# Kernel optimization log

Hardware: AMD Instinct MI355X
Metric: run time of the kernel (lower is better)

## Reference

```python
import jax, jax.numpy as jnp
import numpy as np

H, DH = 16, 64  # heads, dim_head (inner_dim = 1024)
VARIANCE_CONSTANT = 1.0


def setup_inputs() -> dict:
    key = jax.random.key(0)
    ks = jax.random.split(key, 6)
    b, n, m, dim = 8, 4096, 64, 1024
    inner = H * DH
    x = jax.random.normal(ks[0], (b, n, dim), dtype=jnp.float32)
    latents = jax.random.normal(ks[1], (b, m, dim), dtype=jnp.float32)
    mask = jax.random.randint(ks[2], (b, n), 0, 2).astype(bool)  # True = masked out
    sd = 1.0 / np.sqrt(dim)
    Wq = jax.random.normal(ks[3], (inner, dim), dtype=jnp.float32) * sd
    Wkv = jax.random.normal(ks[4], (2 * inner, dim), dtype=jnp.float32) * sd
    Wout = jax.random.normal(ks[5], (dim, inner), dtype=jnp.float32) * sd
    return {"x": x, "latents": latents, "mask": mask, "Wq": Wq, "Wkv": Wkv, "Wout": Wout}


def _split_heads(t):  # b n (h d) -> b h n d
    b, n, _ = t.shape
    return t.reshape(b, n, H, DH).transpose(0, 2, 1, 3)


def reference(x, latents, mask, Wq, Wkv, Wout):
    b, n, dim = x.shape
    scale = DH ** -0.5
    q = latents @ Wq.T                      # b m inner
    k, v = jnp.split(x @ Wkv.T, 2, axis=-1)  # b n inner each
    q = _split_heads(q) * scale             # b h m d
    k = _split_heads(k)                     # b h n d
    v = _split_heads(v)
    sim = jnp.einsum('bhid,bhjd->bhij', q, k)  # b h m n
    max_neg = -jnp.finfo(sim.dtype).max
    sim = jnp.where(mask[:, None, None, :], max_neg, sim)
    sim_new = sim - jax.lax.stop_gradient(sim.max(axis=-1, keepdims=True))
    # cross-query (dim=-2) unbiased variance -> std over latents, shape b h n
    std = jnp.sqrt(jnp.var(sim_new, axis=-2, ddof=1) + 1e-4)
    std = jnp.where(mask[:, None, :], VARIANCE_CONSTANT, std)
    loss_variance = jnp.mean(jax.nn.relu(VARIANCE_CONSTANT - std))
    attn = jax.nn.softmax(sim_new, axis=-1)
    out = jnp.einsum('bhij,bhjd->bhid', attn, v)         # b h m d
    out = out.transpose(0, 2, 1, 3).reshape(b, -1, H * DH)  # b m inner
    out = out @ Wout.T                                    # b m dim
    return out, loss_variance
```

## Files before the change

kernel.cpp:

```cpp
#include <hip/hip_runtime.h>


using u16 = unsigned short;
typedef short bf16x8_t __attribute__((ext_vector_type(8)));
typedef float f32x4_t __attribute__((ext_vector_type(4)));

__device__ __forceinline__ u16 f2bf(float f) {
    union { float f; unsigned u; } v; v.f = f;
    unsigned r = v.u + 0x7fffu + ((v.u >> 16) & 1u);
    return (u16)(r >> 16);
}

template <typename T> __device__ __forceinline__ T cvt_out(float v);
template <> __device__ __forceinline__ float cvt_out<float>(float v) { return v; }
template <> __device__ __forceinline__ u16   cvt_out<u16>(float v)   { return f2bf(v); }

__device__ __forceinline__ void cp16(const void* g, void* l) {
    __builtin_amdgcn_global_load_lds((const __attribute__((address_space(1))) unsigned int*)g,
                                     (__attribute__((address_space(3))) unsigned int*)l, 16, 0, 0);
}

__global__ void cvt_bf16(const float* __restrict__ src, u16* __restrict__ dst,
                         int n4, float scale) {
    int i = blockIdx.x * 256 + threadIdx.x;
    if (i >= n4) return;
    float4 v = ((const float4*)src)[i];
    ushort4 o;
    o.x = f2bf(v.x * scale); o.y = f2bf(v.y * scale);
    o.z = f2bf(v.z * scale); o.w = f2bf(v.w * scale);
    ((ushort4*)dst)[i] = o;
}

template <typename OutT, bool SWIZ>
__global__ __launch_bounds__(256) void gemm_bt(const u16* __restrict__ A,
                                               const u16* __restrict__ B,
                                               OutT* __restrict__ C,
                                               int M, int N, int K) {
    __shared__ __align__(16) u16 As[128 * 64];
    __shared__ __align__(16) u16 Bs[128 * 64];
    const int tid = threadIdx.x;
    const int wid = tid >> 6, lane = tid & 63;
    int bx = blockIdx.x, by = blockIdx.y;
    if (SWIZ) {
        int fid = blockIdx.y * 16 + blockIdx.x;
        int xcd = fid & 7, l = fid >> 3;
        int s = l >> 6, w = l & 63;
        int sm = s & 3, sn = s >> 2;
        by = xcd * 32 + sm * 8 + (w >> 3);
        bx = sn * 8 + (w & 7);
    }
    const int bm = by * 128, bn = bx * 128;
    const int srow = lane >> 3;
    const int scol = ((lane & 7) ^ srow) * 8;
    const int frow = lane & 15;
    const int wr = (wid >> 1) * 64, wc = (wid & 1) * 64;

    f32x4_t acc[4][4];
#pragma unroll
    for (int i = 0; i < 4; ++i)
#pragma unroll
        for (int j = 0; j < 4; ++j) acc[i][j] = (f32x4_t){0.f, 0.f, 0.f, 0.f};

    for (int k0 = 0; k0 < K; k0 += 64) {
#pragma unroll
        for (int t = 0; t < 4; ++t) {
            const int c = wid * 4 + t;
            const int r = c * 8 + srow;
            cp16(A + (size_t)(bm + r) * K + k0 + scol, As + c * 512);
            cp16(B + (size_t)(bn + r) * K + k0 + scol, Bs + c * 512);
        }
        __syncthreads();
#pragma unroll
        for (int ks = 0; ks < 2; ++ks) {
            const int grp = (((ks * 4 + (lane >> 4)) ^ (frow & 7)) * 8);
            bf16x8_t af[4], bfv[4];
#pragma unroll
            for (int i = 0; i < 4; ++i) {
                af[i]  = *(const bf16x8_t*)(As + (wr + i * 16 + frow) * 64 + grp);
                bfv[i] = *(const bf16x8_t*)(Bs + (wc + i * 16 + frow) * 64 + grp);
            }
#pragma unroll
            for (int i = 0; i < 4; ++i)
#pragma unroll
                for (int j = 0; j < 4; ++j)
                    acc[i][j] = __builtin_amdgcn_mfma_f32_16x16x32_bf16(af[i], bfv[j], acc[i][j], 0, 0, 0);
        }
        __syncthreads();
    }
    const int cr = (lane >> 4) * 4, cc = lane & 15;
#pragma unroll
    for (int i = 0; i < 4; ++i)
#pragma unroll
        for (int j = 0; j < 4; ++j) {
            size_t base = (size_t)(bm + wr + i * 16 + cr) * N + (bn + wc + j * 16 + cc);
#pragma unroll
            for (int r = 0; r < 4; ++r)
                C[base + (size_t)r * N] = cvt_out<OutT>(acc[i][j][r]);
        }
}

__global__ __launch_bounds__(256, 1) void attn_max(const u16* __restrict__ q,
                                                   const u16* __restrict__ kv,
                                                   const int* __restrict__ mask,
                                                   float* __restrict__ Mg) {
    const int c = blockIdx.x & 3, bh = blockIdx.x >> 2, b = bh >> 4, h = bh & 15;
    const int tid = threadIdx.x, wid = tid >> 6, lane = tid & 63;
    const int frow = lane & 15, cr = (lane >> 4) * 4;
    const int srow = lane >> 3, scol = ((lane & 7) ^ srow) * 8;

    __shared__ __align__(16) u16 qs[64 * 64];
    __shared__ __align__(16) u16 ks[256 * 64];
    __shared__ float maskf[256];
    __shared__ float Mpart[4][64];

    const size_t kvbase = (size_t)b * 4096 * 2048 + (size_t)h * 64;

#pragma unroll
    for (int t = 0; t < 2; ++t) {
        int cq = wid * 2 + t;
        int r = cq * 8 + srow;
        cp16(q + (size_t)(b * 64 + r) * 1024 + h * 64 + scol, qs + cq * 512);
    }

    float mloc[16];
#pragma unroll
    for (int i = 0; i < 16; ++i) mloc[i] = -3.0e38f;

    for (int sc = 0; sc < 4; ++sc) {
        const int j0 = c * 1024 + sc * 256;
        __syncthreads();
#pragma unroll
        for (int t = 0; t < 8; ++t) {
            int cs = wid * 8 + t;
            int r = cs * 8 + srow;
            cp16(kv + kvbase + (size_t)(j0 + r) * 2048 + scol, ks + cs * 512);
        }
        maskf[tid] = (mask[b * 4096 + j0 + tid] != 0) ? 1.f : 0.f;
        __syncthreads();

        f32x4_t sacc[4][4];
#pragma unroll
        for (int i = 0; i < 4; ++i)
#pragma unroll
            for (int j = 0; j < 4; ++j) sacc[i][j] = (f32x4_t){0.f, 0.f, 0.f, 0.f};
#pragma unroll
        for (int ks2 = 0; ks2 < 2; ++ks2) {
            const int grp = (((ks2 * 4 + (lane >> 4)) ^ (frow & 7)) * 8);
            bf16x8_t af[4], bfv[4];
#pragma unroll
            for (int i = 0; i < 4; ++i) {
                af[i]  = *(const bf16x8_t*)(qs + (i * 16 + frow) * 64 + grp);
                bfv[i] = *(const bf16x8_t*)(ks + (wid * 64 + i * 16 + frow) * 64 + grp);
            }
#pragma unroll
            for (int i = 0; i < 4; ++i)
#pragma unroll
                for (int j = 0; j < 4; ++j)
                    sacc[i][j] = __builtin_amdgcn_mfma_f32_16x16x32_bf16(af[i], bfv[j], sacc[i][j], 0, 0, 0);
        }
#pragma unroll
        for (int nt = 0; nt < 4; ++nt) {
            const int jl = wid * 64 + nt * 16 + frow;
            if (maskf[jl] < 0.5f) {
#pragma unroll
                for (int mt = 0; mt < 4; ++mt)
#pragma unroll
                    for (int r = 0; r < 4; ++r)
                        mloc[mt * 4 + r] = fmaxf(mloc[mt * 4 + r], sacc[mt][nt][r]);
            }
        }
    }
#pragma unroll
    for (int i = 0; i < 16; ++i) {
        float v = mloc[i];
        v = fmaxf(v, __shfl_xor(v, 1)); v = fmaxf(v, __shfl_xor(v, 2));
        v = fmaxf(v, __shfl_xor(v, 4)); v = fmaxf(v, __shfl_xor(v, 8));
        mloc[i] = v;
    }
    if ((lane & 15) == 0) {
#pragma unroll
        for (int mt = 0; mt < 4; ++mt)
#pragma unroll
            for (int r = 0; r < 4; ++r)
                Mpart[wid][mt * 16 + cr + r] = mloc[mt * 4 + r];
    }
    __syncthreads();
    if (tid < 64)
        Mg[(size_t)(bh * 4 + c) * 64 + tid] =
            fmaxf(fmaxf(Mpart[0][tid], Mpart[1][tid]), fmaxf(Mpart[2][tid], Mpart[3][tid]));
}

__global__ __launch_bounds__(256, 1) void attn_pv(const u16* __restrict__ q,
                                                  const u16* __restrict__ kv,
                                                  const int* __restrict__ mask,
                                                  const float* __restrict__ Mg,
                                                  float* __restrict__ Opart,
                                                  float* __restrict__ Rpart,
                                                  float* __restrict__ loss) {
    const int c = blockIdx.x & 3, bh = blockIdx.x >> 2, b = bh >> 4, h = bh & 15;
    const int tid = threadIdx.x, wid = tid >> 6, lane = tid & 63;
    const int frow = lane & 15, cr = (lane >> 4) * 4;
    const int srow = lane >> 3, scol = ((lane & 7) ^ srow) * 8;

    __shared__ __align__(16) u16 qs[64 * 64];
    __shared__ __align__(16) u16 ks[256 * 64];
    __shared__ __align__(16) u16 vt[64 * 256];
    __shared__ float maskf[256];
    __shared__ float Mrow[64];
    __shared__ float RpS[4][64];
    __shared__ float lossP[4];

    const size_t kvbase = (size_t)b * 4096 * 2048 + (size_t)h * 64;

#pragma unroll
    for (int t = 0; t < 2; ++t) {
        int cq = wid * 2 + t;
        int r = cq * 8 + srow;
        cp16(q + (size_t)(b * 64 + r) * 1024 + h * 64 + scol, qs + cq * 512);
    }
    if (tid < 64) {
        float m0 = Mg[(size_t)(bh * 4 + 0) * 64 + tid];
        float m1 = Mg[(size_t)(bh * 4 + 1) * 64 + tid];
        float m2 = Mg[(size_t)(bh * 4 + 2) * 64 + tid];
        float m3 = Mg[(size_t)(bh * 4 + 3) * 64 + tid];
        Mrow[tid] = fmaxf(fmaxf(m0, m1), fmaxf(m2, m3));
    }

    f32x4_t oacc[4][4];
#pragma unroll
    for (int i = 0; i < 4; ++i)
#pragma unroll
        for (int j = 0; j < 4; ++j) oacc[i][j] = (f32x4_t){0.f, 0.f, 0.f, 0.f};
    float rloc[16];
#pragma unroll
    for (int i = 0; i < 16; ++i) rloc[i] = 0.f;
    float lossacc = 0.f;

    for (int sc = 0; sc < 4; ++sc) {
        const int j0 = c * 1024 + sc * 256;
        __syncthreads();
#pragma unroll
        for (int t = 0; t < 8; ++t) {
            int cs = wid * 8 + t;
            int r = cs * 8 + srow;
            cp16(kv + kvbase + (size_t)(j0 + r) * 2048 + scol, ks + cs * 512);
        }
        {
            const u16* vrow = kv + kvbase + 1024 + (size_t)(j0 + tid) * 2048;
            const int jhi = tid >> 3, jlo = tid & 7;
#pragma unroll
            for (int p = 0; p < 8; ++p) {
                bf16x8_t v = *(const bf16x8_t*)(vrow + p * 8);
#pragma unroll
                for (int e = 0; e < 8; ++e) {
                    const int d = p * 8 + e;
                    vt[d * 256 + ((jhi ^ (d & 7)) * 8) + jlo] = (u16)v[e];
                }
            }
        }
        maskf[tid] = (mask[b * 4096 + j0 + tid] != 0) ? 1.f : 0.f;
        __syncthreads();

        f32x4_t sacc[4][4];
#pragma unroll
        for (int i = 0; i < 4; ++i)
#pragma unroll
            for (int j = 0; j < 4; ++j) sacc[i][j] = (f32x4_t){0.f, 0.f, 0.f, 0.f};
#pragma unroll
        for (int ks2 = 0; ks2 < 2; ++ks2) {
            const int grp = (((ks2 * 4 + (lane >> 4)) ^ (frow & 7)) * 8);
            bf16x8_t af[4], bfv[4];
#pragma unroll
            for (int i = 0; i < 4; ++i) {
                af[i]  = *(const bf16x8_t*)(qs + (i * 16 + frow) * 64 + grp);
                bfv[i] = *(const bf16x8_t*)(ks + (wid * 64 + i * 16 + frow) * 64 + grp);
            }
#pragma unroll
            for (int i = 0; i < 4; ++i)
#pragma unroll
                for (int j = 0; j < 4; ++j)
                    sacc[i][j] = __builtin_amdgcn_mfma_f32_16x16x32_bf16(af[i], bfv[j], sacc[i][j], 0, 0, 0);
        }
        __syncthreads();

#pragma unroll
        for (int nt = 0; nt < 4; ++nt) {
            const int jl = wid * 64 + nt * 16 + frow;
            const bool msk = maskf[jl] > 0.5f;
            const int jh = jl >> 3, jlo2 = jl & 7;
            float c1 = 0.f, c2 = 0.f;
#pragma unroll
            for (int mt = 0; mt < 4; ++mt) {
#pragma unroll
                for (int r = 0; r < 4; ++r) {
                    const int row = mt * 16 + cr + r;
                    const float t = sacc[mt][nt][r] - Mrow[row];
                    const float p = msk ? 0.f : __expf(t);
                    rloc[mt * 4 + r] += p;
                    c1 += msk ? 0.f : t;
                    c2 += msk ? 0.f : t * t;
                    ks[row * 256 + ((jh ^ (row & 7)) * 8) + jlo2] = f2bf(p);
                }
            }
            c1 += __shfl_xor(c1, 16); c1 += __shfl_xor(c1, 32);
            c2 += __shfl_xor(c2, 16); c2 += __shfl_xor(c2, 32);
            if (lane < 16 && !msk) {
                const float var = (c2 - c1 * c1 * (1.f / 64.f)) * (1.f / 63.f);
                lossacc += fmaxf(1.f - sqrtf(var + 1e-4f), 0.f);
            }
        }
#pragma unroll
        for (int ks2 = 0; ks2 < 2; ++ks2) {
            bf16x8_t pa[4], vb[4];
#pragma unroll
            for (int i = 0; i < 4; ++i) {
                const int grp = (((wid * 8 + ks2 * 4 + (lane >> 4)) ^ (frow & 7)) * 8);
                pa[i] = *(const bf16x8_t*)(ks + (i * 16 + frow) * 256 + grp);
                vb[i] = *(const bf16x8_t*)(vt + (i * 16 + frow) * 256 + grp);
            }
#pragma unroll
            for (int i = 0; i < 4; ++i)
#pragma unroll
                for (int j = 0; j < 4; ++j)
                    oacc[i][j] = __builtin_amdgcn_mfma_f32_16x16x32_bf16(pa[i], vb[j], oacc[i][j], 0, 0, 0);
        }
    }

    __syncthreads();
    float* Os = (float*)ks;
    for (int i = tid; i < 4096; i += 256) Os[i] = 0.f;
#pragma unroll
    for (int i = 0; i < 16; ++i) {
        float v = rloc[i];
        v += __shfl_xor(v, 1); v += __shfl_xor(v, 2);
        v += __shfl_xor(v, 4); v += __shfl_xor(v, 8);
        rloc[i] = v;
    }
    if ((lane & 15) == 0) {
#pragma unroll
        for (int mt = 0; mt < 4; ++mt)
#pragma unroll
            for (int r = 0; r < 4; ++r)
                RpS[wid][mt * 16 + cr + r] = rloc[mt * 4 + r];
    }
    __syncthreads();
#pragma unroll
    for (int mt = 0; mt < 4; ++mt)
#pragma unroll
        for (int dt = 0; dt < 4; ++dt)
#pragma unroll
            for (int r = 0; r < 4; ++r)
                atomicAdd(&Os[(mt * 16 + cr + r) * 64 + dt * 16 + frow], oacc[mt][dt][r]);
    __syncthreads();
    const size_t ob = (size_t)(bh * 4 + c) * 4096;
    for (int e = tid; e < 4096; e += 256) Opart[ob + e] = Os[e];
    if (tid < 64)
        Rpart[(size_t)(bh * 4 + c) * 64 + tid] =
            RpS[0][tid] + RpS[1][tid] + RpS[2][tid] + RpS[3][tid];

    float v = lossacc;
    v += __shfl_xor(v, 1); v += __shfl_xor(v, 2); v += __shfl_xor(v, 4);
    v += __shfl_xor(v, 8); v += __shfl_xor(v, 16); v += __shfl_xor(v, 32);
    if (lane == 0) lossP[wid] = v;
    __syncthreads();
    if (tid == 0)
        atomicAdd(loss, (lossP[0] + lossP[1] + lossP[2] + lossP[3]) * (1.f / 524288.f));
}

__global__ __launch_bounds__(256) void attn_fin(const float* __restrict__ Opart,
                                                const float* __restrict__ Rpart,
                                                u16* __restrict__ ao) {
    const int bh = blockIdx.x, b = bh >> 4, h = bh & 15;
    const int tid = threadIdx.x;
    __shared__ float Rt[64];
    if (tid < 64) {
        float r = 0.f;
#pragma unroll
        for (int cc = 0; cc < 4; ++cc) r += Rpart[(size_t)(bh * 4 + cc) * 64 + tid];
        Rt[tid] = r;
    }
    __syncthreads();
    for (int e = tid; e < 4096; e += 256) {
        float o = 0.f;
#pragma unroll
        for (int cc = 0; cc < 4; ++cc) o += Opart[(size_t)(bh * 4 + cc) * 4096 + e];
        const int row = e >> 6, d = e & 63;
        ao[(size_t)(b * 64 + row) * 1024 + h * 64 + d] = f2bf(o / Rt[row]);
    }
}

extern "C" void kernel_launch(void* const* d_in, const int* in_sizes, int n_in,
                              void* d_out, int out_size, void* d_ws, size_t ws_size,
                              hipStream_t stream) {
    const float* x    = (const float*)d_in[0];
    const float* lat  = (const float*)d_in[1];
    const int*   mask = (const int*)d_in[2];
    const float* Wq   = (const float*)d_in[3];
    const float* Wkv  = (const float*)d_in[4];
    const float* Wout = (const float*)d_in[5];
    float* out = (float*)d_out;

    char* ws = (char*)d_ws;
    u16* x_bf    = (u16*)(ws);
    u16* kvb     = (u16*)(ws + 67108864);
    u16* wq_bf   = (u16*)(ws + 201326592);
    u16* wkv_bf  = (u16*)(ws + 203423744);
    u16* wout_bf = (u16*)(ws + 207618048);
    u16* lat_bf  = (u16*)(ws + 209715200);
    u16* q_bf    = (u16*)(ws + 210763776);
    u16* ao_bf   = (u16*)(ws + 211812352);
    float* Mg    = (float*)(ws);
    float* Opart = (float*)(ws + 1048576);
    float* Rpart = (float*)(ws + 1048576 + 8388608);

    hipMemsetAsync(out + 524288, 0, 4, stream);

    cvt_bf16<<<32768, 256, 0, stream>>>(x, x_bf, 8388608, 1.f);
    cvt_bf16<<<512, 256, 0, stream>>>(lat, lat_bf, 131072, 1.f);
    cvt_bf16<<<1024, 256, 0, stream>>>(Wq, wq_bf, 262144, 0.125f);
    cvt_bf16<<<2048, 256, 0, stream>>>(Wkv, wkv_bf, 524288, 1.f);
    cvt_bf16<<<1024, 256, 0, stream>>>(Wout, wout_bf, 262144, 1.f);

    dim3 blk(256);
    gemm_bt<u16, false><<<dim3(8, 4), blk, 0, stream>>>(lat_bf, wq_bf, q_bf, 512, 1024, 1024);
    gemm_bt<u16, true><<<dim3(16, 256), blk, 0, stream>>>(x_bf, wkv_bf, kvb, 32768, 2048, 1024);
    attn_max<<<512, blk, 0, stream>>>(q_bf, kvb, mask, Mg);
    attn_pv<<<512, blk, 0, stream>>>(q_bf, kvb, mask, Mg, Opart, Rpart, out + 524288);
    attn_fin<<<128, blk, 0, stream>>>(Opart, Rpart, ao_bf);
    gemm_bt<float, false><<<dim3(8, 4), blk, 0, stream>>>(ao_bf, wout_bf, out, 512, 1024, 1024);
}
```

Baseline: 526.8 us.

## Emit V pre-transposed from projection GEMM, fuse weight casts, smaller tiles for small GEMMs

Splits the KV projection into a K GEMM and a separate V GEMM whose epilogue writes V transposed per head (b,h,d,n) through an LDS staging tile. attn_pv can then load V with async global-to-LDS copies instead of doing a scalar per-element transpose into shared memory. The four small weight and latent conversions are merged into one launch. The q and out GEMMs switch to 64x64 tiles so they launch more blocks. The cost is an extra pass over x_bf for the second GEMM and more LDS in gemm_v.

```diff
diff --git a/kernel.cpp b/kernel.cpp
--- a/kernel.cpp
+++ b/kernel.cpp
@@ -31,7 +31,24 @@
     ((ushort4*)dst)[i] = o;
 }
 
-template <typename OutT, bool SWIZ>
+__global__ void cvt_w(const float* __restrict__ lat, const float* __restrict__ wq,
+                      const float* __restrict__ wkv, const float* __restrict__ wout,
+                      u16* __restrict__ latb, u16* __restrict__ wqb,
+                      u16* __restrict__ wkvb, u16* __restrict__ woutb) {
+    int i = blockIdx.x * 256 + threadIdx.x;
+    const float* s; u16* d; int off; float sc = 1.f;
+    if (i < 131072)      { s = lat;  d = latb;  off = i; }
+    else if (i < 393216) { s = wq;   d = wqb;   off = i - 131072; sc = 0.125f; }
+    else if (i < 917504) { s = wkv;  d = wkvb;  off = i - 393216; }
+    else                 { s = wout; d = woutb; off = i - 917504; }
+    float4 v = ((const float4*)s)[off];
+    ushort4 o;
+    o.x = f2bf(v.x * sc); o.y = f2bf(v.y * sc);
+    o.z = f2bf(v.z * sc); o.w = f2bf(v.w * sc);
+    ((ushort4*)d)[off] = o;
+}
+
+template <typename OutT, int SWIZ>
 __global__ __launch_bounds__(256) void gemm_bt(const u16* __restrict__ A,
                                                const u16* __restrict__ B,
                                                OutT* __restrict__ C,
@@ -41,13 +58,12 @@
     const int tid = threadIdx.x;
     const int wid = tid >> 6, lane = tid & 63;
     int bx = blockIdx.x, by = blockIdx.y;
-    if (SWIZ) {
-        int fid = blockIdx.y * 16 + blockIdx.x;
+    if (SWIZ == 1) {
+        int fid = blockIdx.y * 8 + blockIdx.x;
         int xcd = fid & 7, l = fid >> 3;
         int s = l >> 6, w = l & 63;
-        int sm = s & 3, sn = s >> 2;
-        by = xcd * 32 + sm * 8 + (w >> 3);
-        bx = sn * 8 + (w & 7);
+        by = xcd * 32 + s * 8 + (w >> 3);
+        bx = w & 7;
     }
     const int bm = by * 128, bn = bx * 128;
     const int srow = lane >> 3;
@@ -99,8 +115,143 @@
         }
 }
 
+__global__ __launch_bounds__(256) void gemm_v(const u16* __restrict__ A,
+                                              const u16* __restrict__ B,
+                                              u16* __restrict__ Vt, int K) {
+    __shared__ __align__(16) u16 As[128 * 64];
+    __shared__ __align__(16) u16 Bs[128 * 64];
+    __shared__ __align__(16) u16 Ct[128 * 136];
+    const int tid = threadIdx.x;
+    const int wid = tid >> 6, lane = tid & 63;
+    int fid = blockIdx.y * 8 + blockIdx.x;
+    int xcd = fid & 7, l = fid >> 3;
+    int s = l >> 6, w = l & 63;
+    int by = xcd * 32 + s * 8 + (w >> 3);
+    int bx = w & 7;
+    const int bm = by * 128, bn = bx * 128;
+    const int srow = lane >> 3;
+    const int scol = ((lane & 7) ^ srow) * 8;
+    const int frow = lane & 15;
+    const int wr = (wid >> 1) * 64, wc = (wid & 1) * 64;
+
+    f32x4_t acc[4][4];
+#pragma unroll
+    for (int i = 0; i < 4; ++i)
+#pragma unroll
+        for (int j = 0; j < 4; ++j) acc[i][j] = (f32x4_t){0.f, 0.f, 0.f, 0.f};
+
+    for (int k0 = 0; k0 < K; k0 += 64) {
+#pragma unroll
+        for (int t = 0; t < 4; ++t) {
+            const int c = wid * 4 + t;
+            const int r = c * 8 + srow;
+            cp16(A + (size_t)(bm + r) * K + k0 + scol, As + c * 512);
+            cp16(B + (size_t)(bn + r) * K + k0 + scol, Bs + c * 512);
+        }
+        __syncthreads();
+#pragma unroll
+        for (int ks = 0; ks < 2; ++ks) {
+            const int grp = (((ks * 4 + (lane >> 4)) ^ (frow & 7)) * 8);
+            bf16x8_t af[4], bfv[4];
+#pragma unroll
+            for (int i = 0; i < 4; ++i) {
+                af[i]  = *(const bf16x8_t*)(As + (wr + i * 16 + frow) * 64 + grp);
+                bfv[i] = *(const bf16x8_t*)(Bs + (wc + i * 16 + frow) * 64 + grp);
+            }
+#pragma unroll
+            for (int i = 0; i < 4; ++i)
+#pragma unroll
+                for (int j = 0; j < 4; ++j)
+                    acc[i][j] = __builtin_amdgcn_mfma_f32_16x16x32_bf16(af[i], bfv[j], acc[i][j], 0, 0, 0);
+        }
+        __syncthreads();
+    }
+    const int cr = (lane >> 4) * 4, cc = lane & 15;
+#pragma unroll
+    for (int i = 0; i < 4; ++i)
+#pragma unroll
+        for (int j = 0; j < 4; ++j) {
+            const int vdl = wc + j * 16 + cc;
+            const int jl = wr + i * 16 + cr;
+            ushort4 pk;
+            pk.x = f2bf(acc[i][j][0]); pk.y = f2bf(acc[i][j][1]);
+            pk.z = f2bf(acc[i][j][2]); pk.w = f2bf(acc[i][j][3]);
+            *(ushort4*)(Ct + vdl * 136 + jl) = pk;
+        }
+    __syncthreads();
+    const int b = bm >> 12, jb = bm & 4095, vd0 = bn;
+#pragma unroll
+    for (int p = 0; p < 8; ++p) {
+        const int vdl = p * 16 + (tid >> 4);
+        const int jl = (tid & 15) * 8;
+        bf16x8_t v = *(const bf16x8_t*)(Ct + vdl * 136 + jl);
+        const int vd = vd0 + vdl;
+        const size_t addr = ((size_t)(b * 16 + (vd >> 6)) * 64 + (vd & 63)) * 4096 + jb + jl;
+        *(bf16x8_t*)(Vt + addr) = v;
+    }
+}
+
+template <typename OutT>
+__global__ __launch_bounds__(256) void gemm_bt64(const u16* __restrict__ A,
+                                                 const u16* __restrict__ B,
+                                                 OutT* __restrict__ C,
+                                                 int M, int N, int K) {
+    __shared__ __align__(16) u16 As[64 * 64];
+    __shared__ __align__(16) u16 Bs[64 * 64];
+    const int tid = threadIdx.x;
+    const int wid = tid >> 6, lane = tid & 63;
+    const int bm = blockIdx.y * 64, bn = blockIdx.x * 64;
+    const int srow = lane >> 3;
+    const int scol = ((lane & 7) ^ srow) * 8;
+    const int frow = lane & 15;
+    const int wr = (wid >> 1) * 32, wc = (wid & 1) * 32;
+
+    f32x4_t acc[2][2];
+#pragma unroll
+    for (int i = 0; i < 2; ++i)
+#pragma unroll
+        for (int j = 0; j < 2; ++j) acc[i][j] = (f32x4_t){0.f, 0.f, 0.f, 0.f};
+
+    for (int k0 = 0; k0 < K; k0 += 64) {
+#pragma unroll
+        for (int t = 0; t < 2; ++t) {
+            const int c = wid * 2 + t;
+            const int r = c * 8 + srow;
+            cp16(A + (size_t)(bm + r) * K + k0 + scol, As + c * 512);
+            cp16(B + (size_t)(bn + r) * K + k0 + scol, Bs + c * 512);
+        }
+        __syncthreads();
+#pragma unroll
+        for (int ks = 0; ks < 2; ++ks) {
+            const int grp = (((ks * 4 + (lane >> 4)) ^ (frow & 7)) * 8);
+            bf16x8_t af[2], bfv[2];
+#pragma unroll
+            for (int i = 0; i < 2; ++i) {
+                af[i]  = *(const bf16x8_t*)(As + (wr + i * 16 + frow) * 64 + grp);
+                bfv[i] = *(const bf16x8_t*)(Bs + (wc + i * 16 + frow) * 64 + grp);
+            }
+#pragma unroll
+            for (int i = 0; i < 2; ++i)
+#pragma unroll
+                for (int j = 0; j < 2; ++j)
+                    acc[i][j] = __builtin_amdgcn_mfma_f32_16x16x32_bf16(af[i], bfv[j], acc[i][j], 0, 0, 0);
+        }
+        __syncthreads();
+    }
+    const int cr = (lane >> 4) * 4, cc = lane & 15;
+#pragma unroll
+    for (int i = 0; i < 2; ++i)
+#pragma unroll
+        for (int j = 0; j < 2; ++j) {
+            size_t base = (size_t)(bm + wr + i * 16 + cr) * N + (bn + wc + j * 16 + cc);
+#pragma unroll
+            for (int r = 0; r < 4; ++r)
+                C[base + (size_t)r * N] = cvt_out<OutT>(acc[i][j][r]);
+        }
+}
+
 __global__ __launch_bounds__(256, 1) void attn_max(const u16* __restrict__ q,
-                                                   const u16* __restrict__ kv,
+                                                   const u16* __restrict__ kbuf,
                                                    const int* __restrict__ mask,
                                                    float* __restrict__ Mg) {
     const int c = blockIdx.x & 3, bh = blockIdx.x >> 2, b = bh >> 4, h = bh & 15;
@@ -113,7 +264,7 @@
     __shared__ float maskf[256];
     __shared__ float Mpart[4][64];
 
-    const size_t kvbase = (size_t)b * 4096 * 2048 + (size_t)h * 64;
+    const size_t kbase = (size_t)b * 4096 * 1024 + (size_t)h * 64;
 
 #pragma unroll
     for (int t = 0; t < 2; ++t) {
@@ -133,7 +284,7 @@
         for (int t = 0; t < 8; ++t) {
             int cs = wid * 8 + t;
             int r = cs * 8 + srow;
-            cp16(kv + kvbase + (size_t)(j0 + r) * 2048 + scol, ks + cs * 512);
+            cp16(kbuf + kbase + (size_t)(j0 + r) * 1024 + scol, ks + cs * 512);
         }
         maskf[tid] = (mask[b * 4096 + j0 + tid] != 0) ? 1.f : 0.f;
         __syncthreads();
@@ -191,7 +342,8 @@
 }
 
 __global__ __launch_bounds__(256, 1) void attn_pv(const u16* __restrict__ q,
-                                                  const u16* __restrict__ kv,
+                                                  const u16* __restrict__ kbuf,
+                                                  const u16* __restrict__ vtbuf,
                                                   const int* __restrict__ mask,
                                                   const float* __restrict__ Mg,
                                                   float* __restrict__ Opart,
@@ -204,13 +356,14 @@
 
     __shared__ __align__(16) u16 qs[64 * 64];
     __shared__ __align__(16) u16 ks[256 * 64];
-    __shared__ __align__(16) u16 vt[64 * 256];
+    __shared__ __align__(16) u16 vts[64 * 256];
     __shared__ float maskf[256];
     __shared__ float Mrow[64];
     __shared__ float RpS[4][64];
     __shared__ float lossP[4];
 
-    const size_t kvbase = (size_t)b * 4096 * 2048 + (size_t)h * 64;
+    const size_t kbase = (size_t)b * 4096 * 1024 + (size_t)h * 64;
+    const size_t vtbase = (size_t)bh * 64 * 4096;
 
 #pragma unroll
     for (int t = 0; t < 2; ++t) {
@@ -243,20 +396,15 @@
         for (int t = 0; t < 8; ++t) {
             int cs = wid * 8 + t;
             int r = cs * 8 + srow;
-            cp16(kv + kvbase + (size_t)(j0 + r) * 2048 + scol, ks + cs * 512);
-        }
-        {
-            const u16* vrow = kv + kvbase + 1024 + (size_t)(j0 + tid) * 2048;
-            const int jhi = tid >> 3, jlo = tid & 7;
-#pragma unroll
-            for (int p = 0; p < 8; ++p) {
-                bf16x8_t v = *(const bf16x8_t*)(vrow + p * 8);
-#pragma unroll
-                for (int e = 0; e < 8; ++e) {
-                    const int d = p * 8 + e;
-                    vt[d * 256 + ((jhi ^ (d & 7)) * 8) + jlo] = (u16)v[e];
-                }
-            }
+            cp16(kbuf + kbase + (size_t)(j0 + r) * 1024 + scol, ks + cs * 512);
+        }
+#pragma unroll
+        for (int t = 0; t < 8; ++t) {
+            int cs = wid * 8 + t;
+            int r = cs * 2 + (lane >> 5);
+            int gs = lane & 31;
+            cp16(vtbuf + vtbase + (size_t)r * 4096 + j0 + ((gs ^ (r & 7)) * 8),
+                 vts + cs * 512);
         }
         maskf[tid] = (mask[b * 4096 + j0 + tid] != 0) ? 1.f : 0.f;
         __syncthreads();
@@ -316,7 +464,7 @@
             for (int i = 0; i < 4; ++i) {
                 const int grp = (((wid * 8 + ks2 * 4 + (lane >> 4)) ^ (frow & 7)) * 8);
                 pa[i] = *(const bf16x8_t*)(ks + (i * 16 + frow) * 256 + grp);
-                vb[i] = *(const bf16x8_t*)(vt + (i * 16 + frow) * 256 + grp);
+                vb[i] = *(const bf16x8_t*)(vts + (i * 16 + frow) * 256 + grp);
             }
 #pragma unroll
             for (int i = 0; i < 4; ++i)
@@ -402,7 +550,8 @@
 
     char* ws = (char*)d_ws;
     u16* x_bf    = (u16*)(ws);
-    u16* kvb     = (u16*)(ws + 67108864);
+    u16* kbuf    = (u16*)(ws + 67108864);
+    u16* vtbuf   = (u16*)(ws + 134217728);
     u16* wq_bf   = (u16*)(ws + 201326592);
     u16* wkv_bf  = (u16*)(ws + 203423744);
     u16* wout_bf = (u16*)(ws + 207618048);
@@ -416,16 +565,14 @@
     hipMemsetAsync(out + 524288, 0, 4, stream);
 
     cvt_bf16<<<32768, 256, 0, stream>>>(x, x_bf, 8388608, 1.f);
-    cvt_bf16<<<512, 256, 0, stream>>>(lat, lat_bf, 131072, 1.f);
-    cvt_bf16<<<1024, 256, 0, stream>>>(Wq, wq_bf, 262144, 0.125f);
-    cvt_bf16<<<2048, 256, 0, stream>>>(Wkv, wkv_bf, 524288, 1.f);
-    cvt_bf16<<<1024, 256, 0, stream>>>(Wout, wout_bf, 262144, 1.f);
+    cvt_w<<<4608, 256, 0, stream>>>(lat, Wq, Wkv, Wout, lat_bf, wq_bf, wkv_bf, wout_bf);
 
     dim3 blk(256);
-    gemm_bt<u16, false><<<dim3(8, 4), blk, 0, stream>>>(lat_bf, wq_bf, q_bf, 512, 1024, 1024);
-    gemm_bt<u16, true><<<dim3(16, 256), blk, 0, stream>>>(x_bf, wkv_bf, kvb, 32768, 2048, 1024);
-    attn_max<<<512, blk, 0, stream>>>(q_bf, kvb, mask, Mg);
-    attn_pv<<<512, blk, 0, stream>>>(q_bf, kvb, mask, Mg, Opart, Rpart, out + 524288);
+    gemm_bt64<u16><<<dim3(16, 8), blk, 0, stream>>>(lat_bf, wq_bf, q_bf, 512, 1024, 1024);
+    gemm_bt<u16, 1><<<dim3(8, 256), blk, 0, stream>>>(x_bf, wkv_bf, kbuf, 32768, 1024, 1024);
+    gemm_v<<<dim3(8, 256), blk, 0, stream>>>(x_bf, wkv_bf + 1024 * 1024, vtbuf, 1024);
+    attn_max<<<512, blk, 0, stream>>>(q_bf, kbuf, mask, Mg);
+    attn_pv<<<512, blk, 0, stream>>>(q_bf, kbuf, vtbuf, mask, Mg, Opart, Rpart, out + 524288);
     attn_fin<<<128, blk, 0, stream>>>(Opart, Rpart, ao_bf);
-    gemm_bt<float, false><<<dim3(8, 4), blk, 0, stream>>>(ao_bf, wout_bf, out, 512, 1024, 1024);
-}
+    gemm_bt64<float><<<dim3(16, 8), blk, 0, stream>>>(ao_bf, wout_bf, out, 512, 1024, 1024);
+}
```

Result: no change. 518.9 us (-1.5%).
